# Kernel tuning notes

Hardware: AMD Instinct MI355X
Metric: run time of the kernel (lower is better)

## Reference

```python
import jax, jax.numpy as jnp
import numpy as np

D_MODEL = 1024
N_HEADS = 16
DH = D_MODEL // N_HEADS
ROPE_THETA = 10000.0


def rotate_half(u):
    h = u.shape[-1] // 2
    return jnp.concatenate([-u[..., h:], u[..., :h]], axis=-1)


def apply_rope(q, k, cos, sin):
    return q * cos + rotate_half(q) * sin, k * cos + rotate_half(k) * sin


def setup_inputs() -> dict:
    key = jax.random.key(0)
    ks = jax.random.split(key, 6)
    B, S = 2, 2048
    x = jax.random.normal(ks[0], (B, S, D_MODEL), dtype=jnp.float32)
    y = jax.random.normal(ks[1], (B, S, D_MODEL), dtype=jnp.float32)
    wq = 0.01 * jax.random.normal(ks[2], (D_MODEL, D_MODEL), dtype=jnp.float32)
    wk = 0.01 * jax.random.normal(ks[3], (D_MODEL, D_MODEL), dtype=jnp.float32)
    wv = 0.01 * jax.random.normal(ks[4], (D_MODEL, D_MODEL), dtype=jnp.float32)
    wo = 0.01 * jax.random.normal(ks[5], (D_MODEL, D_MODEL), dtype=jnp.float32)
    return {"x": x, "y": y, "wq": wq, "wk": wk, "wv": wv, "wo": wo}


def reference(x, y, wq, wk, wv, wo):
    B, S, D = x.shape
    past_length = 0  # default; kv_cache=None

    Q = x @ wq.T                      # (B,S,D)
    K = y                             # NOTE: K is y un-projected (as in source)
    V = y @ wv.T
    # K1 = x @ wk.T is computed in the source but immediately overwritten
    # by the buggy second apply_rope call -> wk is unused in the output.
    V1 = x @ wo.T

    def heads(t):
        return t.reshape(B, S, N_HEADS, DH).transpose(0, 2, 1, 3)  # (B,H,S,dh)

    q_h, k_h, v_h, v1_h = heads(Q), heads(K), heads(V), heads(V1)

    # RoPE tables (past_length:past_length+S rows of the cache)
    freqs = 1.0 / ROPE_THETA ** (jnp.arange(0, DH, 2, dtype=jnp.float32) / DH)
    emb = jnp.arange(past_length, past_length + S, dtype=jnp.float32)[:, None] * freqs[None, :]
    cos = jnp.concatenate([jnp.cos(emb), jnp.cos(emb)], axis=-1)[None, None]  # (1,1,S,dh)
    sin = jnp.concatenate([jnp.sin(emb), jnp.sin(emb)], axis=-1)[None, None]

    q_h, k_h = apply_rope(q_h, k_h, cos, sin)
    # faithful to source: k1 = rope applied AGAIN to the already-roped k
    _, k1_h = apply_rope(q_h, k_h, cos, sin)

    k_full = jnp.concatenate([k_h, k1_h], axis=2)   # (B,H,2S,dh)
    v_full = jnp.concatenate([v_h, v1_h], axis=2)
    S_full = k_full.shape[2]

    # mask: tril(diagonal=past_length) over (S,S_full), last S cols = eye(S)
    rows = jnp.arange(S)[:, None]
    cols = jnp.arange(S_full)[None, :]
    mask = cols <= rows + past_length
    mask = mask.at[:, -S:].set(jnp.eye(S, dtype=bool))  # (S,S_full)

    scores = jnp.einsum("bhqd,bhkd->bhqk", q_h, k_full) / jnp.sqrt(jnp.asarray(DH, x.dtype))
    scores = jnp.where(mask[None, None], scores, jnp.asarray(-1e30, x.dtype))
    attn = jax.nn.softmax(scores, axis=-1)
    out = jnp.einsum("bhqk,bhkd->bhqd", attn, v_full)
    out = out.transpose(0, 2, 1, 3).reshape(B, S, D)

    k_ret = k_full[:, :, :-S, :]
    return out, k_ret
```

## Files before the change

kernel.cpp:

```cpp
#include <hip/hip_runtime.h>

#define DM 1024
#define NHEADS 16
#define DHEAD 64
#define BB 2
#define SS 2048
#define BH (BB*NHEADS)

typedef __attribute__((ext_vector_type(8))) short short8;
typedef __attribute__((ext_vector_type(4))) float float4v;
typedef unsigned short ushort_t;

#define LN1E4_D32 0.28782313662425572f

static __device__ __forceinline__ unsigned short f2bf(float f) {
    union { float f; unsigned u; } v; v.f = f;
    unsigned r = v.u + 0x7fffu + ((v.u >> 16) & 1u);
    return (unsigned short)(r >> 16);
}
static __device__ __forceinline__ float bf2f(unsigned short u) {
    union { float f; unsigned u; } v; v.u = ((unsigned)u) << 16;
    return v.f;
}
static __device__ __forceinline__ unsigned cvtpk_bf16(float lo, float hi) {
    unsigned r;
    asm("v_cvt_pk_bf16_f32 %0, %1, %2" : "=v"(r) : "v"(lo), "v"(hi));
    return r;
}

static __device__ __forceinline__ void gload16(const ushort_t* g, ushort_t* l) {
    __builtin_amdgcn_global_load_lds(
        (const __attribute__((address_space(1))) void*)g,
        (__attribute__((address_space(3))) void*)l, 16, 0, 0);
}

__global__ __launch_bounds__(256) void cvt_tile_kernel(
        const float* __restrict__ x, const float* __restrict__ wq,
        const float* __restrict__ wv, const float* __restrict__ wo,
        ushort_t* __restrict__ xb, ushort_t* __restrict__ wqb,
        ushort_t* __restrict__ wvb, ushort_t* __restrict__ wob) {
    int C = blockIdx.x * 256 + threadIdx.x;
    int c  = C & 511;
    int tl = C >> 9;
    int rb = tl >> 5, kb = tl & 31;
    const float* src; ushort_t* dst; int r0;
    if (rb < 32)      { src = x;  r0 = rb * 128;        dst = xb  + (size_t)tl * 4096; }
    else if (rb < 40) { src = wq; r0 = (rb - 32) * 128; dst = wqb + (size_t)(((rb - 32) * 32) + kb) * 4096; }
    else if (rb < 48) { src = wv; r0 = (rb - 40) * 128; dst = wvb + (size_t)(((rb - 40) * 32) + kb) * 4096; }
    else              { src = wo; r0 = (rb - 48) * 128; dst = wob + (size_t)(((rb - 48) * 32) + kb) * 4096; }
    int row = c >> 2, g = c & 3;
    int kk3 = g ^ ((row >> 1) & 3);
    const float* s = src + (size_t)(r0 + row) * DM + kb * 32 + kk3 * 8;
    float4 a0 = *reinterpret_cast<const float4*>(s);
    float4 a1 = *reinterpret_cast<const float4*>(s + 4);
    short8 v;
    v[0] = (short)f2bf(a0.x); v[1] = (short)f2bf(a0.y);
    v[2] = (short)f2bf(a0.z); v[3] = (short)f2bf(a0.w);
    v[4] = (short)f2bf(a1.x); v[5] = (short)f2bf(a1.y);
    v[6] = (short)f2bf(a1.z); v[7] = (short)f2bf(a1.w);
    *reinterpret_cast<short8*>(dst + c * 8) = v;
}

__global__ __launch_bounds__(256) void rope_k_kernel(const float* __restrict__ y,
        float* __restrict__ kout, ushort_t* __restrict__ khb, ushort_t* __restrict__ yb) {
    int t = blockIdx.x * blockDim.x + threadIdx.x;
    int i8 = t & 3;
    int s  = (t >> 2) & (SS - 1);
    int bh = t >> 13;
    int h = bh & (NHEADS - 1), b = bh >> 4;

    const float* yp = y + ((size_t)(b * SS + s)) * DM + h * DHEAD + i8 * 8;
    float4 a0 = *reinterpret_cast<const float4*>(yp);
    float4 a1 = *reinterpret_cast<const float4*>(yp + 4);
    float4 b0 = *reinterpret_cast<const float4*>(yp + 32);
    float4 b1 = *reinterpret_cast<const float4*>(yp + 36);
    float u0[8] = {a0.x, a0.y, a0.z, a0.w, a1.x, a1.y, a1.z, a1.w};
    float u1[8] = {b0.x, b0.y, b0.z, b0.w, b1.x, b1.y, b1.z, b1.w};
    float lo[8], hi[8];
#pragma unroll
    for (int j = 0; j < 8; j++) {
        int i = i8 * 8 + j;
        float freq = __expf(-(float)i * LN1E4_D32);
        float th = (float)s * freq;
        float cv = cosf(th), sv = sinf(th);
        lo[j] = u0[j] * cv - u1[j] * sv;
        hi[j] = u1[j] * cv + u0[j] * sv;
    }
    float* op = kout + ((size_t)bh * SS + s) * DHEAD + i8 * 8;
    *reinterpret_cast<float4*>(op)      = (float4){lo[0], lo[1], lo[2], lo[3]};
    *reinterpret_cast<float4*>(op + 4)  = (float4){lo[4], lo[5], lo[6], lo[7]};
    *reinterpret_cast<float4*>(op + 32) = (float4){hi[0], hi[1], hi[2], hi[3]};
    *reinterpret_cast<float4*>(op + 36) = (float4){hi[4], hi[5], hi[6], hi[7]};

    ushort_t* kb = khb + ((size_t)bh * 32 + (s >> 6)) * 4096 + (s & 63) * 64;
    short8 vlo, vhi;
#pragma unroll
    for (int j = 0; j < 8; j++) { vlo[j] = (short)f2bf(lo[j]); vhi[j] = (short)f2bf(hi[j]); }
    *reinterpret_cast<short8*>(kb + ((i8 ^ (s & 7)) << 3))       = vlo;
    *reinterpret_cast<short8*>(kb + (((i8 + 4) ^ (s & 7)) << 3)) = vhi;

    int rowm = b * SS + s;
    int rowin = rowm & 127, rbm = rowm >> 7;
    int g = i8 ^ ((rowin >> 1) & 3);
    ushort_t* yt = yb + ((size_t)(rbm * 32 + h * 2)) * 4096 + rowin * 32 + (g << 3);
    short8 ulo, uhi;
#pragma unroll
    for (int j = 0; j < 8; j++) { ulo[j] = (short)f2bf(u0[j]); uhi[j] = (short)f2bf(u1[j]); }
    *reinterpret_cast<short8*>(yt)        = ulo;
    *reinterpret_cast<short8*>(yt + 4096) = uhi;
}

__global__ __launch_bounds__(256, 2) void gemm3_kernel(
        const ushort_t* __restrict__ xb, const ushort_t* __restrict__ yb,
        const ushort_t* __restrict__ wqb, const ushort_t* __restrict__ wvb,
        const ushort_t* __restrict__ wob,
        ushort_t* __restrict__ qh, ushort_t* __restrict__ vt, ushort_t* __restrict__ v1h) {
    __shared__ __align__(16) char smem[34816];
    ushort_t* As = (ushort_t*)smem;
    ushort_t* Bs = (ushort_t*)(smem + 16384);
    ushort_t (*Ct)[136] = (ushort_t(*)[136])smem;

    int bid = blockIdx.x;
    int xcd = bid & 7;
    int s_  = bid >> 3;
    int zo  = s_ >> 5;
    int z   = (zo == 0) ? 0 : (zo == 1 ? 2 : 1);
    int t_  = s_ & 31;
    int n0  = (t_ >> 2) * 128;
    int m0  = (xcd * 4 + (t_ & 3)) * 128;

    const ushort_t* A = (z == 1) ? yb : xb;
    const ushort_t* W = (z == 0) ? wqb : (z == 1 ? wvb : wob);
    ushort_t* O = (z == 0) ? qh : (z == 1 ? vt : v1h);

    const ushort_t* Atl = A + (size_t)(m0 >> 7) * 32 * 4096;
    const ushort_t* Wtl = W + (size_t)(n0 >> 7) * 32 * 4096;

    int tid = threadIdx.x;
    int wave = tid >> 6, lane = tid & 63, quad = lane >> 4, l15 = lane & 15;
    int wr = (wave >> 1) * 64, wc = (wave & 1) * 64;

    int gi0 = tid * 8, gi1 = (256 + tid) * 8;
    int li0 = (tid & 192) * 8, li1 = (256 + (tid & 192)) * 8;

    int aoff[4], boff[4];
#pragma unroll
    for (int mi = 0; mi < 4; mi++) {
        int row = wr + mi * 16 + l15;
        aoff[mi] = row * 32 + ((quad ^ ((row >> 1) & 3)) << 3);
    }
#pragma unroll
    for (int ni = 0; ni < 4; ni++) {
        int row = wc + ni * 16 + l15;
        boff[ni] = row * 32 + ((quad ^ ((row >> 1) & 3)) << 3);
    }

    float4v acc[4][4];
#pragma unroll
    for (int a = 0; a < 4; a++)
#pragma unroll
        for (int b = 0; b < 4; b++)
            acc[a][b] = (float4v){0.f, 0.f, 0.f, 0.f};

    gload16(Atl + gi0, As + li0); gload16(Atl + gi1, As + li1);
    gload16(Wtl + gi0, Bs + li0); gload16(Wtl + gi1, Bs + li1);
    int cur = 0;

    for (int kb = 0; kb < 32; kb++) {
        __syncthreads();
        if (kb + 1 < 32) {
            const ushort_t* at = Atl + (size_t)(kb + 1) * 4096;
            const ushort_t* wt = Wtl + (size_t)(kb + 1) * 4096;
            int nb = (cur ^ 1) * 4096;
            gload16(at + gi0, As + nb + li0); gload16(at + gi1, As + nb + li1);
            gload16(wt + gi0, Bs + nb + li0); gload16(wt + gi1, Bs + nb + li1);
        }
        const ushort_t* Ac = As + cur * 4096;
        const ushort_t* Bc = Bs + cur * 4096;
        short8 af[4], bfr[4];
#pragma unroll
        for (int mi = 0; mi < 4; mi++)
            af[mi] = *reinterpret_cast<const short8*>(&Ac[aoff[mi]]);
#pragma unroll
        for (int ni = 0; ni < 4; ni++)
            bfr[ni] = *reinterpret_cast<const short8*>(&Bc[boff[ni]]);
#pragma unroll
        for (int mi = 0; mi < 4; mi++)
#pragma unroll
            for (int ni = 0; ni < 4; ni++)
                acc[mi][ni] = __builtin_amdgcn_mfma_f32_16x16x32_bf16(af[mi], bfr[ni], acc[mi][ni], 0, 0, 0);
        cur ^= 1;
    }

    if (z == 0) {
#pragma unroll
        for (int mi = 0; mi < 4; mi++)
#pragma unroll
            for (int r = 0; r < 4; r++) {
                int m = m0 + wr + mi * 16 + quad * 4 + r;
                float pos = (float)(m & (SS - 1));
#pragma unroll
                for (int ni = 0; ni < 2; ni++) {
                    int d = ni * 16 + l15;
                    float f = __expf(-(float)d * LN1E4_D32);
                    float th = pos * f;
                    float cv, sv;
                    __sincosf(th, &sv, &cv);
                    float u0 = acc[mi][ni][r], u1 = acc[mi][ni + 2][r];
                    acc[mi][ni][r]     = u0 * cv - u1 * sv;
                    acc[mi][ni + 2][r] = u1 * cv + u0 * sv;
                }
            }
    }

    __syncthreads();
#pragma unroll
    for (int mi = 0; mi < 4; mi++)
#pragma unroll
        for (int ni = 0; ni < 4; ni++) {
            int col = wc + ni * 16 + l15;
#pragma unroll
            for (int r = 0; r < 4; r++)
                Ct[wr + mi * 16 + quad * 4 + r][col] = f2bf(acc[mi][ni][r]);
        }
    __syncthreads();
    int h0 = n0 >> 6;
    if (z == 1) {
        int b = m0 >> 11;
        int s0 = m0 & (SS - 1);
#pragma unroll
        for (int it = 0; it < 8; it++) {
            int c = it * 256 + tid;
            int dh  = c & 63;
            int k16 = (c >> 6) & 15;
            int hh  = c >> 10;
            short8 v;
#pragma unroll
            for (int e = 0; e < 8; e++)
                v[e] = (short)Ct[k16 * 8 + e][hh * 64 + dh];
            int kt = (s0 >> 6) + (k16 >> 3);
            size_t off = ((size_t)((b * NHEADS + h0 + hh) * 32 + kt)) * 4096
                       + dh * 64 + (((k16 & 7) ^ (dh & 7)) << 3);
            *reinterpret_cast<short8*>(&O[off]) = v;
        }
    } else {
#pragma unroll
        for (int it = 0; it < 8; it++) {
            int c = it * 256 + tid;
            int o = c >> 3, j = c & 7;
            int hh = o >> 7, mr = o & 127;
            int m = m0 + mr, b = m >> 11, si = m & (SS - 1);
            uint4 v = *reinterpret_cast<const uint4*>(&Ct[mr][hh * 64 + j * 8]);
            *reinterpret_cast<uint4*>(
                &O[((size_t)((b * NHEADS + h0 + hh) * SS + si)) * DHEAD + j * 8]) = v;
        }
    }
}

template<bool MASKED>
static __device__ __forceinline__ void attn_tile(
        const ushort_t* __restrict__ Kc, const ushort_t* __restrict__ Vc, int kbase,
        int quad, int l15, int q0w, const short8* qf,
        ushort_t (*Psw)[70], float4v* Oa, float& lsum) {
    float4v sa[4];
#pragma unroll
    for (int t2 = 0; t2 < 4; t2++) sa[t2] = (float4v){0.f, 0.f, 0.f, 0.f};
#pragma unroll
    for (int t2 = 0; t2 < 4; t2++) {
        int key = t2 * 16 + l15;
        int ro = key * 64, sw = key & 7;
#pragma unroll
        for (int half = 0; half < 2; half++) {
            short8 kf = *reinterpret_cast<const short8*>(&Kc[ro + (((half * 4 + quad) ^ sw) << 3)]);
            sa[t2] = __builtin_amdgcn_mfma_f32_16x16x32_bf16(kf, qf[half], sa[t2], 0, 0, 0);
        }
    }
    int query = q0w + l15;
#pragma unroll
    for (int t2 = 0; t2 < 4; t2++) {
        float p[4];
#pragma unroll
        for (int r = 0; r < 4; r++) {
            float e = __expf(sa[t2][r] * 0.125f);
            if (MASKED) {
                int key = kbase + t2 * 16 + quad * 4 + r;
                p[r] = (key <= query) ? e : 0.f;
            } else {
                p[r] = e;
            }
        }
        lsum += (p[0] + p[1]) + (p[2] + p[3]);
        unsigned w0 = cvtpk_bf16(p[0], p[1]);
        unsigned w1 = cvtpk_bf16(p[2], p[3]);
        *reinterpret_cast<unsigned*>(&Psw[l15][t2 * 16 + quad * 4])     = w0;
        *reinterpret_cast<unsigned*>(&Psw[l15][t2 * 16 + quad * 4 + 2]) = w1;
    }
    short8 pf0 = *reinterpret_cast<const short8*>(&Psw[l15][quad * 8]);
    short8 pf1 = *reinterpret_cast<const short8*>(&Psw[l15][32 + quad * 8]);
#pragma unroll
    for (int t = 0; t < 4; t++) {
        int dh = t * 16 + l15;
        int ro = dh * 64, sw = dh & 7;
        short8 vf0 = *reinterpret_cast<const short8*>(&Vc[ro + ((quad ^ sw) << 3)]);
        short8 vf1 = *reinterpret_cast<const short8*>(&Vc[ro + (((4 + quad) ^ sw) << 3)]);
        Oa[t] = __builtin_amdgcn_mfma_f32_16x16x32_bf16(pf0, vf0, Oa[t], 0, 0, 0);
        Oa[t] = __builtin_amdgcn_mfma_f32_16x16x32_bf16(pf1, vf1, Oa[t], 0, 0, 0);
    }
}

__global__ __launch_bounds__(256, 2) void attn_kernel(
        const ushort_t* __restrict__ qh, const float* __restrict__ kf32,
        const ushort_t* __restrict__ khb, const ushort_t* __restrict__ vtb,
        const ushort_t* __restrict__ v1h, float* __restrict__ out) {
    __shared__ __align__(16) ushort_t Ks[2][4096];
    __shared__ __align__(16) ushort_t Vt[2][4096];
    __shared__ ushort_t Ps[4][16][70];
    __shared__ float sdiag[4][16];
    __shared__ float sred[4][16];

    int bid = blockIdx.x;
    int bh = (bid & 7) * 4 + ((bid >> 3) & 3);
    int qb = 31 - (bid >> 5);
    int q0 = qb * 64;

    int tid = threadIdx.x, wave = tid >> 6, lane = tid & 63, quad = lane >> 4, l15 = lane & 15;
    int q0w = q0 + wave * 16;
    const ushort_t* qp  = qh  + (size_t)bh * SS * DHEAD;
    const float*    kp  = kf32 + (size_t)bh * SS * DHEAD;
    const ushort_t* v1p = v1h + (size_t)bh * SS * DHEAD;
    const ushort_t* ktb = khb + (size_t)bh * 32 * 4096;
    const ushort_t* vtt = vtb + (size_t)bh * 32 * 4096;

    short8 qf[2];
    qf[0] = *reinterpret_cast<const short8*>(&qp[(q0w + l15) * DHEAD + quad * 8]);
    qf[1] = *reinterpret_cast<const short8*>(&qp[(q0w + l15) * DHEAD + 32 + quad * 8]);

    float4v Oa[4];
#pragma unroll
    for (int t = 0; t < 4; t++) Oa[t] = (float4v){0.f, 0.f, 0.f, 0.f};
    float lsum = 0.f;

    int gi0 = tid * 8, gi1 = (256 + tid) * 8;
    int li0 = (tid & 192) * 8, li1 = (256 + (tid & 192)) * 8;

    gload16(ktb + gi0, &Ks[0][li0]); gload16(ktb + gi1, &Ks[0][li1]);
    gload16(vtt + gi0, &Vt[0][li0]); gload16(vtt + gi1, &Vt[0][li1]);
    int cur = 0;

    for (int kt = 0; kt < qb; kt++) {
        __syncthreads();
        const ushort_t* gk = ktb + (size_t)(kt + 1) * 4096;
        const ushort_t* gv = vtt + (size_t)(kt + 1) * 4096;
        int nb = cur ^ 1;
        gload16(gk + gi0, &Ks[nb][li0]); gload16(gk + gi1, &Ks[nb][li1]);
        gload16(gv + gi0, &Vt[nb][li0]); gload16(gv + gi1, &Vt[nb][li1]);
        attn_tile<false>(Ks[cur], Vt[cur], kt * 64, quad, l15, q0w, qf, Ps[wave], Oa, lsum);
        cur ^= 1;
    }
    __syncthreads();
    attn_tile<true>(Ks[cur], Vt[cur], qb * 64, quad, l15, q0w, qf, Ps[wave], Oa, lsum);

    lsum += __shfl_xor(lsum, 16);
    lsum += __shfl_xor(lsum, 32);
    if (quad == 0) sred[wave][l15] = lsum;

    {
        int sk = q0w + l15;
        const float* krow = kp + (size_t)sk * DHEAD;
        short8 k1lo, k1hi;
#pragma unroll
        for (int j = 0; j < 8; j++) {
            int d = quad * 8 + j;
            float f = __expf(-(float)d * LN1E4_D32);
            float th = (float)sk * f;
            float cv, sv;
            __sincosf(th, &sv, &cv);
            float a = krow[d], b2 = krow[d + 32];
            k1lo[j] = (short)f2bf(a * cv - b2 * sv);
            k1hi[j] = (short)f2bf(b2 * cv + a * sv);
        }
        float4v sd4 = (float4v){0.f, 0.f, 0.f, 0.f};
        sd4 = __builtin_amdgcn_mfma_f32_16x16x32_bf16(qf[0], k1lo, sd4, 0, 0, 0);
        sd4 = __builtin_amdgcn_mfma_f32_16x16x32_bf16(qf[1], k1hi, sd4, 0, 0, 0);
#pragma unroll
        for (int r = 0; r < 4; r++)
            if (l15 == quad * 4 + r) sdiag[wave][l15] = sd4[r] * 0.125f;
        __syncthreads();

        int b = bh >> 4, h = bh & (NHEADS - 1);
#pragma unroll
        for (int r = 0; r < 4; r++) {
            float ls = sred[wave][quad * 4 + r];
            float pd = __expf(sdiag[wave][quad * 4 + r]);
            int query = q0w + quad * 4 + r;
            float linv = 1.f / (ls + pd);
#pragma unroll
            for (int t = 0; t < 4; t++) {
                float v1v = bf2f(v1p[query * DHEAD + t * 16 + l15]);
                float o = (Oa[t][r] + pd * v1v) * linv;
                out[(b * SS + query) * DM + h * DHEAD + t * 16 + l15] = o;
            }
        }
    }
}

extern "C" void kernel_launch(void* const* d_in, const int* in_sizes, int n_in,
                              void* d_out, int out_size, void* d_ws, size_t ws_size,
                              hipStream_t stream) {
    const float* x  = (const float*)d_in[0];
    const float* y  = (const float*)d_in[1];
    const float* wq = (const float*)d_in[2];
    const float* wv = (const float*)d_in[4];
    const float* wo = (const float*)d_in[5];
    float* outp  = (float*)d_out;
    float* k_out = outp + (size_t)BB * SS * DM;

    char* ws = (char*)d_ws;
    ushort_t* vtb = (ushort_t*)(ws);
    ushort_t* v1b = (ushort_t*)(ws + (8ull  << 20));
    ushort_t* qhb = (ushort_t*)(ws + (16ull << 20));
    ushort_t* khb = (ushort_t*)(ws + (24ull << 20));
    ushort_t* xb  = (ushort_t*)(ws + (32ull << 20));
    ushort_t* yb  = (ushort_t*)(ws + (40ull << 20));
    ushort_t* wqb = (ushort_t*)(ws + (48ull << 20));
    ushort_t* wvb = (ushort_t*)(ws + (50ull << 20));
    ushort_t* wob = (ushort_t*)(ws + (52ull << 20));

    cvt_tile_kernel<<<3584, 256, 0, stream>>>(x, wq, wv, wo, xb, wqb, wvb, wob);
    rope_k_kernel<<<1024, 256, 0, stream>>>(y, k_out, khb, yb);
    gemm3_kernel<<<768, 256, 0, stream>>>(xb, yb, wqb, wvb, wob, qhb, vtb, v1b);
    attn_kernel<<<1024, 256, 0, stream>>>(qhb, k_out, khb, vtb, v1b, outp);
}
```

Before: 176.1 us.

## Use 128-query attention blocks with 8 waves and XOR-swizzled P staging

The attention kernel now processes 128 queries per block with 512 threads (8 waves), so each K/V tile loaded into shared memory is reused by twice as many queries and the grid halves. Waves skip key tiles entirely above their causal range and choose the masked or unmasked path per tile. The per-wave P scratch changes from padded 70-wide rows to 64-wide rows with an XOR swizzle to avoid bank conflicts. In exchange, waves within a block now have unbalanced causal work at the diagonal, there are fewer blocks for load balance, and register pressure rises under the 512-thread launch bound.

```diff
diff --git a/kernel.cpp b/kernel.cpp
--- a/kernel.cpp
+++ b/kernel.cpp
@@ -261,7 +261,7 @@
 static __device__ __forceinline__ void attn_tile(
         const ushort_t* __restrict__ Kc, const ushort_t* __restrict__ Vc, int kbase,
         int quad, int l15, int q0w, const short8* qf,
-        ushort_t (*Psw)[70], float4v* Oa, float& lsum) {
+        ushort_t* __restrict__ Psw, float4v* Oa, float& lsum) {
     float4v sa[4];
 #pragma unroll
     for (int t2 = 0; t2 < 4; t2++) sa[t2] = (float4v){0.f, 0.f, 0.f, 0.f};
@@ -276,6 +276,7 @@
         }
     }
     int query = q0w + l15;
+    int swl = l15 & 7;
 #pragma unroll
     for (int t2 = 0; t2 < 4; t2++) {
         float p[4];
@@ -292,11 +293,12 @@
         lsum += (p[0] + p[1]) + (p[2] + p[3]);
         unsigned w0 = cvtpk_bf16(p[0], p[1]);
         unsigned w1 = cvtpk_bf16(p[2], p[3]);
-        *reinterpret_cast<unsigned*>(&Psw[l15][t2 * 16 + quad * 4])     = w0;
-        *reinterpret_cast<unsigned*>(&Psw[l15][t2 * 16 + quad * 4 + 2]) = w1;
-    }
-    short8 pf0 = *reinterpret_cast<const short8*>(&Psw[l15][quad * 8]);
-    short8 pf1 = *reinterpret_cast<const short8*>(&Psw[l15][32 + quad * 8]);
+        int chunk = (((t2 * 2 + (quad >> 1)) ^ swl) << 3) + (quad & 1) * 4;
+        *reinterpret_cast<unsigned*>(&Psw[l15 * 64 + chunk])     = w0;
+        *reinterpret_cast<unsigned*>(&Psw[l15 * 64 + chunk + 2]) = w1;
+    }
+    short8 pf0 = *reinterpret_cast<const short8*>(&Psw[l15 * 64 + ((quad ^ swl) << 3)]);
+    short8 pf1 = *reinterpret_cast<const short8*>(&Psw[l15 * 64 + (((4 + quad) ^ swl) << 3)]);
 #pragma unroll
     for (int t = 0; t < 4; t++) {
         int dh = t * 16 + l15;
@@ -308,20 +310,20 @@
     }
 }
 
-__global__ __launch_bounds__(256, 2) void attn_kernel(
+__global__ __launch_bounds__(512, 2) void attn_kernel(
         const ushort_t* __restrict__ qh, const float* __restrict__ kf32,
         const ushort_t* __restrict__ khb, const ushort_t* __restrict__ vtb,
         const ushort_t* __restrict__ v1h, float* __restrict__ out) {
     __shared__ __align__(16) ushort_t Ks[2][4096];
     __shared__ __align__(16) ushort_t Vt[2][4096];
-    __shared__ ushort_t Ps[4][16][70];
-    __shared__ float sdiag[4][16];
-    __shared__ float sred[4][16];
+    __shared__ __align__(16) ushort_t Ps[8][16][64];
+    __shared__ float sdiag[8][16];
+    __shared__ float sred[8][16];
 
     int bid = blockIdx.x;
     int bh = (bid & 7) * 4 + ((bid >> 3) & 3);
-    int qb = 31 - (bid >> 5);
-    int q0 = qb * 64;
+    int jq = 15 - (bid >> 5);
+    int q0 = jq * 128;
 
     int tid = threadIdx.x, wave = tid >> 6, lane = tid & 63, quad = lane >> 4, l15 = lane & 15;
     int q0w = q0 + wave * 16;
@@ -340,25 +342,34 @@
     for (int t = 0; t < 4; t++) Oa[t] = (float4v){0.f, 0.f, 0.f, 0.f};
     float lsum = 0.f;
 
-    int gi0 = tid * 8, gi1 = (256 + tid) * 8;
-    int li0 = (tid & 192) * 8, li1 = (256 + (tid & 192)) * 8;
-
-    gload16(ktb + gi0, &Ks[0][li0]); gload16(ktb + gi1, &Ks[0][li1]);
-    gload16(vtt + gi0, &Vt[0][li0]); gload16(vtt + gi1, &Vt[0][li1]);
+    int gi = tid * 8;
+    int li = (tid & 448) * 8;
+
+    int ntiles = jq * 2 + 2;
+    gload16(ktb + gi, &Ks[0][li]);
+    gload16(vtt + gi, &Vt[0][li]);
     int cur = 0;
 
-    for (int kt = 0; kt < qb; kt++) {
+    for (int kt = 0; kt < ntiles; kt++) {
         __syncthreads();
-        const ushort_t* gk = ktb + (size_t)(kt + 1) * 4096;
-        const ushort_t* gv = vtt + (size_t)(kt + 1) * 4096;
-        int nb = cur ^ 1;
-        gload16(gk + gi0, &Ks[nb][li0]); gload16(gk + gi1, &Ks[nb][li1]);
-        gload16(gv + gi0, &Vt[nb][li0]); gload16(gv + gi1, &Vt[nb][li1]);
-        attn_tile<false>(Ks[cur], Vt[cur], kt * 64, quad, l15, q0w, qf, Ps[wave], Oa, lsum);
+        if (kt + 1 < ntiles) {
+            const ushort_t* gk = ktb + (size_t)(kt + 1) * 4096;
+            const ushort_t* gv = vtt + (size_t)(kt + 1) * 4096;
+            int nb = cur ^ 1;
+            gload16(gk + gi, &Ks[nb][li]);
+            gload16(gv + gi, &Vt[nb][li]);
+        }
+        int kbase = kt * 64;
+        if (kbase <= q0w + 15) {
+            if (kbase + 63 <= q0w)
+                attn_tile<false>(Ks[cur], Vt[cur], kbase, quad, l15, q0w, qf,
+                                 &Ps[wave][0][0], Oa, lsum);
+            else
+                attn_tile<true>(Ks[cur], Vt[cur], kbase, quad, l15, q0w, qf,
+                                &Ps[wave][0][0], Oa, lsum);
+        }
         cur ^= 1;
     }
-    __syncthreads();
-    attn_tile<true>(Ks[cur], Vt[cur], qb * 64, quad, l15, q0w, qf, Ps[wave], Oa, lsum);
 
     lsum += __shfl_xor(lsum, 16);
     lsum += __shfl_xor(lsum, 32);
@@ -429,5 +440,5 @@
     cvt_tile_kernel<<<3584, 256, 0, stream>>>(x, wq, wv, wo, xb, wqb, wvb, wob);
     rope_k_kernel<<<1024, 256, 0, stream>>>(y, k_out, khb, yb);
     gemm3_kernel<<<768, 256, 0, stream>>>(xb, yb, wqb, wvb, wob, qhb, vtb, v1b);
-    attn_kernel<<<1024, 256, 0, stream>>>(qhb, k_out, khb, vtb, v1b, outp);
-}
+    attn_kernel<<<512, 512, 0, stream>>>(qhb, k_out, khb, vtb, v1b, outp);
+}
```

New measurement: 176.0 us. No clear change (-0.1%).
